# Kernel tuning notes

Hardware: AMD Instinct MI355X
Metric: run time of the kernel (lower is better)

The kernel has to match this reference:

```python
import jax, jax.numpy as jnp
import numpy as np

# dims
B, L = 2, 1024            # batch, seq len (queries == keys)
DQ, DK, DSRC = 1024, 1024, 512
VIEWS, WIDTH, TOPK = 8, 4, 8
DVP = DQ // VIEWS         # per-view head dim = 128
PAD_F = (WIDTH - 1) // 2  # dilocal 'same' zero padding (stride=1, dilation=1)
PAD_B = (WIDTH - 1) - PAD_F


def setup_inputs() -> dict:
    key = jax.random.key(0)
    ks = jax.random.split(key, 5)
    s = 0.02
    return {
        "query": jax.random.normal(ks[0], (B, L, DQ), jnp.float32),
        "key_t": jax.random.normal(ks[1], (B, L, DK), jnp.float32),
        "source": jax.random.normal(ks[2], (B, L, DSRC), jnp.float32),
        "wq": jax.random.normal(ks[3], (VIEWS, DVP, DQ), jnp.float32) * s,
        "bq": jnp.zeros((VIEWS, DVP), jnp.float32),
        "wk": jax.random.normal(ks[4], (VIEWS, DVP, DK), jnp.float32) * s,
        "bk": jnp.zeros((VIEWS, DVP), jnp.float32),
    }


def reference(query, key_t, source, wq, bq, wk, bk):
    # --- ViewPointFactory.forward ---
    # multi-view projections: [B, L, D] -> [B, views, L, dvp]
    q = jnp.einsum('bld,vkd->bvlk', query, wq) + bq[None, :, None, :]
    k = jnp.einsum('bld,vkd->bvlk', key_t, wk) + bk[None, :, None, :]
    # attention scores over all keys: [B, views, Lq, Lk] (no sqrt(d) scaling in source)
    score = jnp.einsum('bvqd,bvkd->bvqk', q, k)
    # torch.sort(descending) + slice == top_k with sorted values
    vals, idx = jax.lax.top_k(score, TOPK)          # [B, views, Lq, TOPK]
    weights = jax.nn.softmax(vals, axis=-1)

    # --- ViewPoint.__call__(source) ---
    # dilocal: width-WIDTH local windows, stride 1, dilation 1, zero 'same' pad
    padded = jnp.pad(source, ((0, 0), (PAD_F, PAD_B), (0, 0)))
    win_idx = jnp.arange(L)[:, None] + jnp.arange(WIDTH)[None, :]  # [L, WIDTH]
    windows = padded[:, win_idx, :]                 # [B, L, WIDTH, DSRC]

    # gather the top-k key windows per (view, query): [B, views, Lq, TOPK, WIDTH, DSRC]
    gathered = jax.vmap(lambda w, i: w[i])(windows, idx)
    # weighted sum over top-k -> [B, views, Lq, WIDTH, DSRC]
    out = jnp.einsum('bvqk,bvqkwd->bvqwd', weights, gathered)
    return out
```

## Files before the change

kernel.cpp:

```cpp
#include <hip/hip_runtime.h>
#include <cstdint>

#define L_SEQ 1024
#define DSRC 512
#define XPL 2097152L
#define WPL 1048576L

typedef __attribute__((ext_vector_type(8))) short short8;
typedef __attribute__((ext_vector_type(4))) float floatx4;

__device__ __forceinline__ unsigned short f2bf(float f) {
  unsigned int x = __float_as_uint(f);
  x += 0x7fff + ((x >> 16) & 1);
  return (unsigned short)(x >> 16);
}
__device__ __forceinline__ float bf2f(unsigned short h) {
  return __uint_as_float((unsigned)h << 16);
}
__device__ __forceinline__ void split3(float f, unsigned short* h) {
  h[0] = f2bf(f);
  float d = f - bf2f(h[0]);
  h[1] = f2bf(d);
  h[2] = f2bf(d - bf2f(h[1]));
}

__device__ __forceinline__ void gload_lds16(const void* g, void* l) {
  __builtin_amdgcn_global_load_lds(
      (const __attribute__((address_space(1))) unsigned int*)g,
      (__attribute__((address_space(3))) unsigned int*)l, 16, 0, 0);
}

__global__ __launch_bounds__(256) void split_inputs_k(
    const float* __restrict__ query, const float* __restrict__ key_t,
    const float* __restrict__ wq, const float* __restrict__ wk,
    ushort* __restrict__ xs, ushort* __restrict__ wsp) {
  int blk = blockIdx.x;
  const float* in; ushort* out; long pl; int idx;
  if (blk < 2048)      { in = query; out = xs;           pl = XPL; idx = blk; }
  else if (blk < 4096) { in = key_t; out = xs + 3 * XPL; pl = XPL; idx = blk - 2048; }
  else if (blk < 5120) { in = wq;    out = wsp;          pl = WPL; idx = blk - 4096; }
  else                 { in = wk;    out = wsp + 3 * WPL; pl = WPL; idx = blk - 5120; }
  long e = (long)idx * 1024 + threadIdx.x * 4;
  float4 v = *(const float4*)(in + e);
  unsigned short h0[3], h1[3], h2[3], h3[3];
  split3(v.x, h0); split3(v.y, h1); split3(v.z, h2); split3(v.w, h3);
#pragma unroll
  for (int s = 0; s < 3; s++) {
    ushort4 u; u.x = h0[s]; u.y = h1[s]; u.z = h2[s]; u.w = h3[s];
    *(ushort4*)(out + s * pl + e) = u;
  }
}

__global__ __launch_bounds__(512, 2) void proj_gemm_k(
    const ushort* __restrict__ xs, const ushort* __restrict__ wsp,
    ushort* __restrict__ qs, ushort* __restrict__ ks,
    const float* __restrict__ bq, const float* __restrict__ bk) {
  __shared__ ushort As[2][3][4096];
  __shared__ ushort Bs[2][3][4096];
  int z = blockIdx.z;
  const ushort* Ab = xs + (long)z * 3 * XPL + (long)blockIdx.y * 128 * 1024;
  const ushort* Bb = wsp + (long)z * 3 * WPL + (long)blockIdx.x * 128 * 1024;

  int tid = threadIdx.x;
  int lane = tid & 63, wv = tid >> 6;
  int wm = wv >> 2, wn = wv & 3;
  int quad = lane >> 4, l16 = lane & 15;

  int sr = tid >> 2;
  int scq = (((tid & 3) ^ ((sr >> 1) & 3)) << 3);

  floatx4 acc[4][2] = {};

#pragma unroll
  for (int s = 0; s < 3; s++) {
    gload_lds16(Ab + (long)s * XPL + (long)sr * 1024 + scq, &As[0][s][wv * 512]);
    gload_lds16(Bb + (long)s * WPL + (long)sr * 1024 + scq, &Bs[0][s][wv * 512]);
  }
  __syncthreads();

  int cur = 0;
#pragma unroll 2
  for (int t = 0; t < 32; t++) {
    if (t < 31) {
      int k0 = (t + 1) * 32;
#pragma unroll
      for (int s = 0; s < 3; s++) {
        gload_lds16(Ab + (long)s * XPL + (long)sr * 1024 + k0 + scq, &As[cur ^ 1][s][wv * 512]);
        gload_lds16(Bb + (long)s * WPL + (long)sr * 1024 + k0 + scq, &Bs[cur ^ 1][s][wv * 512]);
      }
    }
    short8 af[3][4];
#pragma unroll
    for (int s = 0; s < 3; s++)
#pragma unroll
      for (int i = 0; i < 4; i++) {
        int row = wm * 64 + i * 16 + l16;
        int qa = (quad ^ ((row >> 1) & 3)) << 3;
        af[s][i] = *(const short8*)(&As[cur][s][row * 32 + qa]);
      }
#pragma unroll
    for (int j = 0; j < 2; j++) {
      int rowb = wn * 32 + j * 16 + l16;
      int boff = rowb * 32 + ((quad ^ ((rowb >> 1) & 3)) << 3);
      short8 b0 = *(const short8*)(&Bs[cur][0][boff]);
      short8 b1 = *(const short8*)(&Bs[cur][1][boff]);
      short8 b2 = *(const short8*)(&Bs[cur][2][boff]);
#pragma unroll
      for (int i = 0; i < 4; i++) {
        acc[i][j] = __builtin_amdgcn_mfma_f32_16x16x32_bf16(af[1][i], b1, acc[i][j], 0, 0, 0);
        acc[i][j] = __builtin_amdgcn_mfma_f32_16x16x32_bf16(af[0][i], b2, acc[i][j], 0, 0, 0);
        acc[i][j] = __builtin_amdgcn_mfma_f32_16x16x32_bf16(af[2][i], b0, acc[i][j], 0, 0, 0);
        acc[i][j] = __builtin_amdgcn_mfma_f32_16x16x32_bf16(af[0][i], b1, acc[i][j], 0, 0, 0);
        acc[i][j] = __builtin_amdgcn_mfma_f32_16x16x32_bf16(af[1][i], b0, acc[i][j], 0, 0, 0);
        acc[i][j] = __builtin_amdgcn_mfma_f32_16x16x32_bf16(af[0][i], b0, acc[i][j], 0, 0, 0);
      }
    }
    __syncthreads();
    cur ^= 1;
  }

  ushort* Ob = z ? ks : qs;
  const float* bias = z ? bk : bq;
#pragma unroll
  for (int j = 0; j < 2; j++) {
    int col = blockIdx.x * 128 + wn * 32 + j * 16 + l16;
    float bv = bias[col];
#pragma unroll
    for (int i = 0; i < 4; i++) {
#pragma unroll
      for (int r = 0; r < 4; r++) {
        long row = blockIdx.y * 128 + wm * 64 + i * 16 + quad * 4 + r;
        float val = acc[i][j][r] + bv;
        unsigned short h[3]; split3(val, h);
        long e = row * 1024 + col;
#pragma unroll
        for (int s = 0; s < 3; s++) Ob[s * XPL + e] = h[s];
      }
    }
  }
}

__global__ __launch_bounds__(512, 4) void score_gemm_k(
    const ushort* __restrict__ qs, const ushort* __restrict__ ks,
    float* __restrict__ S, int b) {
  __shared__ ushort As[3][4096];
  __shared__ ushort Bs[3][4096];
  int v = blockIdx.z;
  const ushort* Ab = qs + (long)b * 1048576 + v * 128 + (long)blockIdx.y * 131072;
  const ushort* Bb = ks + (long)b * 1048576 + v * 128 + (long)blockIdx.x * 131072;

  int tid = threadIdx.x;
  int lane = tid & 63, wv = tid >> 6;
  int wm = wv >> 2, wn = wv & 3;
  int quad = lane >> 4, l16 = lane & 15;

  int sr = tid >> 2;
  int scq = (((tid & 3) ^ ((sr >> 1) & 3)) << 3);

  floatx4 acc[4][2] = {};

  for (int t = 0; t < 4; t++) {
    int k0 = t * 32;
#pragma unroll
    for (int s = 0; s < 3; s++) {
      gload_lds16(Ab + (long)s * XPL + (long)sr * 1024 + k0 + scq, &As[s][wv * 512]);
      gload_lds16(Bb + (long)s * XPL + (long)sr * 1024 + k0 + scq, &Bs[s][wv * 512]);
    }
    __syncthreads();

    short8 af[3][4];
#pragma unroll
    for (int s = 0; s < 3; s++)
#pragma unroll
      for (int i = 0; i < 4; i++) {
        int row = wm * 64 + i * 16 + l16;
        int qa = (quad ^ ((row >> 1) & 3)) << 3;
        af[s][i] = *(const short8*)(&As[s][row * 32 + qa]);
      }
#pragma unroll
    for (int j = 0; j < 2; j++) {
      int rowb = wn * 32 + j * 16 + l16;
      int boff = rowb * 32 + ((quad ^ ((rowb >> 1) & 3)) << 3);
      short8 b0 = *(const short8*)(&Bs[0][boff]);
      short8 b1 = *(const short8*)(&Bs[1][boff]);
      short8 b2 = *(const short8*)(&Bs[2][boff]);
#pragma unroll
      for (int i = 0; i < 4; i++) {
        acc[i][j] = __builtin_amdgcn_mfma_f32_16x16x32_bf16(af[1][i], b1, acc[i][j], 0, 0, 0);
        acc[i][j] = __builtin_amdgcn_mfma_f32_16x16x32_bf16(af[0][i], b2, acc[i][j], 0, 0, 0);
        acc[i][j] = __builtin_amdgcn_mfma_f32_16x16x32_bf16(af[2][i], b0, acc[i][j], 0, 0, 0);
        acc[i][j] = __builtin_amdgcn_mfma_f32_16x16x32_bf16(af[0][i], b1, acc[i][j], 0, 0, 0);
        acc[i][j] = __builtin_amdgcn_mfma_f32_16x16x32_bf16(af[1][i], b0, acc[i][j], 0, 0, 0);
        acc[i][j] = __builtin_amdgcn_mfma_f32_16x16x32_bf16(af[0][i], b0, acc[i][j], 0, 0, 0);
      }
    }
    __syncthreads();
  }

  float* Sb = S + (long)v * 1048576;
#pragma unroll
  for (int j = 0; j < 2; j++) {
    int col = blockIdx.x * 128 + wn * 32 + j * 16 + l16;
#pragma unroll
    for (int i = 0; i < 4; i++) {
#pragma unroll
      for (int r = 0; r < 4; r++) {
        int row = blockIdx.y * 128 + wm * 64 + i * 16 + quad * 4 + r;
        Sb[(long)row * 1024 + col] = acc[i][j][r];
      }
    }
  }
}

__global__ __launch_bounds__(256) void topk_softmax_k(const float* __restrict__ scores,
                                                      float* __restrict__ wts,
                                                      int* __restrict__ idxs) {
  int row = blockIdx.x * 4 + (threadIdx.x >> 6);
  int lane = threadIdx.x & 63;
  const float4* s4 = (const float4*)(scores + (long)row * 1024);
  float v[16];
#pragma unroll
  for (int i = 0; i < 4; i++) {
    float4 t4 = s4[i * 64 + lane];
    v[i * 4 + 0] = t4.x; v[i * 4 + 1] = t4.y; v[i * 4 + 2] = t4.z; v[i * 4 + 3] = t4.w;
  }
  float topv[8]; int topi[8];
  for (int t = 0; t < 8; t++) {
    float bv = -1e30f; int bi = 1 << 30; int bslot = -1;
#pragma unroll
    for (int i = 0; i < 16; i++) {
      int ci = ((i >> 2) << 8) + (lane << 2) + (i & 3);
      if (v[i] > bv) { bv = v[i]; bi = ci; bslot = i; }
    }
    float rv = bv; int ri = bi;
    for (int off = 32; off; off >>= 1) {
      float ov = __shfl_down(rv, off);
      int oi = __shfl_down(ri, off);
      if (ov > rv || (ov == rv && oi < ri)) { rv = ov; ri = oi; }
    }
    rv = __shfl(rv, 0); ri = __shfl(ri, 0);
    topv[t] = rv; topi[t] = ri;
    if (bslot >= 0 && bi == ri) v[bslot] = -1e30f;
  }
  float m = topv[0], sum = 0.f, e[8];
#pragma unroll
  for (int t = 0; t < 8; t++) { e[t] = __expf(topv[t] - m); sum += e[t]; }
  float inv = 1.0f / sum;
  if (lane < 8) {
    wts[(long)row * 8 + lane] = e[lane] * inv;
    idxs[(long)row * 8 + lane] = topi[lane];
  }
}

__global__ __launch_bounds__(256) void gather_out_k(const float* __restrict__ src,
                                                    const float* __restrict__ wts,
                                                    const int* __restrict__ idxs,
                                                    float* __restrict__ out) {
  int rowid = blockIdx.x;
  int b = rowid >> 13;
  int tid = threadIdx.x;
  int d4 = tid & 127;
  int w0 = (tid >> 7) << 1;
  const float4* s4 = (const float4*)src + (long)b * (L_SEQ * (DSRC / 4));
  float wt[8]; int id[8];
#pragma unroll
  for (int k = 0; k < 8; k++) {
    wt[k] = wts[(long)rowid * 8 + k];
    id[k] = idxs[(long)rowid * 8 + k];
  }
  float ax = 0, ay = 0, az = 0, aw = 0;
  float bx = 0, by = 0, bz2 = 0, bw = 0;
#pragma unroll
  for (int k = 0; k < 8; k++) {
    int r0 = id[k] + w0 - 1;
    if ((unsigned)r0 < (unsigned)L_SEQ) {
      float4 x = s4[(long)r0 * 128 + d4];
      ax += wt[k] * x.x; ay += wt[k] * x.y; az += wt[k] * x.z; aw += wt[k] * x.w;
    }
    int r1 = r0 + 1;
    if ((unsigned)r1 < (unsigned)L_SEQ) {
      float4 x = s4[(long)r1 * 128 + d4];
      bx += wt[k] * x.x; by += wt[k] * x.y; bz2 += wt[k] * x.z; bw += wt[k] * x.w;
    }
  }
  float4* o4 = (float4*)out + ((long)rowid * 4 + w0) * 128 + d4;
  o4[0] = make_float4(ax, ay, az, aw);
  o4[128] = make_float4(bx, by, bz2, bw);
}

extern "C" void kernel_launch(void* const* d_in, const int* in_sizes, int n_in,
                              void* d_out, int out_size, void* d_ws, size_t ws_size,
                              hipStream_t stream) {
  (void)in_sizes; (void)n_in; (void)out_size; (void)ws_size;
  const float* query  = (const float*)d_in[0];
  const float* key_t  = (const float*)d_in[1];
  const float* source = (const float*)d_in[2];
  const float* wq     = (const float*)d_in[3];
  const float* bq     = (const float*)d_in[4];
  const float* wk     = (const float*)d_in[5];
  const float* bk     = (const float*)d_in[6];

  char* ws = (char*)d_ws;
  ushort* qs  = (ushort*)(ws);
  ushort* ksp = (ushort*)(ws + 12582912);
  float*  wts = (float*)(ws + 25165824);
  int*    idxs= (int*)(ws + 25690112);
  ushort* xs  = (ushort*)(ws + 26214400);
  ushort* wsp = (ushort*)(ws + 51380224);
  float*  sc  = (float*)(ws + 26214400);

  split_inputs_k<<<6144, 256, 0, stream>>>(query, key_t, wq, wk, xs, wsp);
  proj_gemm_k<<<dim3(8, 16, 2), 512, 0, stream>>>(xs, wsp, qs, ksp, bq, bk);
  for (int b = 0; b < 2; b++) {
    score_gemm_k<<<dim3(8, 8, 8), 512, 0, stream>>>(qs, ksp, sc, b);
    topk_softmax_k<<<2048, 256, 0, stream>>>(sc, wts + (long)b * 65536, idxs + b * 65536);
  }
  gather_out_k<<<16384, 256, 0, stream>>>(source, wts, idxs, (float*)d_out);
}
```

Measured before the change: 328.8 us.

## Fuse score GEMM with streaming top-k softmax, avoiding score matrix round-trip

Replaces the per-batch score GEMM plus separate top-k/softmax kernels with one kernel. Each block keeps a 64-row query tile resident in LDS and streams key tiles through a double-buffered LDS stage. After each 128-column tile it keeps a running top-8 per row via shuffle merges, so the full 8x1024x1024 fp32 score matrix is never written to or read from global memory. Blocks are mapped to XCDs by (batch, view) pair. The cost is fewer, heavier blocks (256 total), larger LDS use, and serial top-k merge work interleaved between MFMA phases.

```diff
diff --git a/kernel.cpp b/kernel.cpp
--- a/kernel.cpp
+++ b/kernel.cpp
@@ -140,116 +140,170 @@
   }
 }
 
-__global__ __launch_bounds__(512, 4) void score_gemm_k(
+__global__ __launch_bounds__(512) void score_topk_k(
     const ushort* __restrict__ qs, const ushort* __restrict__ ks,
-    float* __restrict__ S, int b) {
-  __shared__ ushort As[3][4096];
-  __shared__ ushort Bs[3][4096];
-  int v = blockIdx.z;
-  const ushort* Ab = qs + (long)b * 1048576 + v * 128 + (long)blockIdx.y * 131072;
-  const ushort* Bb = ks + (long)b * 1048576 + v * 128 + (long)blockIdx.x * 131072;
+    float* __restrict__ wts, int* __restrict__ idxs) {
+  __shared__ ushort Asm[3 * 64 * 128];
+  __shared__ ushort Bsm[2][3 * 128 * 32];
+  __shared__ float  Ssm[64 * 132];
+
+  int fid = blockIdx.x + 16 * (blockIdx.y + 8 * blockIdx.z);
+  int xcd = fid & 7, jj = fid >> 3;
+  int pair = xcd * 2 + (jj & 1);
+  int rt = jj >> 1;
+  int v = pair & 7, b = pair >> 3;
+
+  const long arow0 = (long)b * 1024 + rt * 64;
+  const long brow0 = (long)b * 1024;
+  const int vb = v * 128;
 
   int tid = threadIdx.x;
   int lane = tid & 63, wv = tid >> 6;
   int wm = wv >> 2, wn = wv & 3;
   int quad = lane >> 4, l16 = lane & 15;
 
-  int sr = tid >> 2;
-  int scq = (((tid & 3) ^ ((sr >> 1) & 3)) << 3);
-
-  floatx4 acc[4][2] = {};
-
-  for (int t = 0; t < 4; t++) {
-    int k0 = t * 32;
-#pragma unroll
-    for (int s = 0; s < 3; s++) {
-      gload_lds16(Ab + (long)s * XPL + (long)sr * 1024 + k0 + scq, &As[s][wv * 512]);
-      gload_lds16(Bb + (long)s * XPL + (long)sr * 1024 + k0 + scq, &Bs[s][wv * 512]);
-    }
+#pragma unroll
+  for (int n = 0; n < 6; n++) {
+    int base = n * 512 + wv * 64;
+    int sl = base + lane;
+    int s = sl >> 10, rem = sl & 1023;
+    int r = rem >> 4, sq = rem & 15;
+    int qb = sq ^ (r & 7);
+    gload_lds16(qs + (long)s * XPL + (arow0 + r) * 1024 + vb + qb * 8,
+                &Asm[base * 8]);
+  }
+
+  auto stageB = [&](int step, int bsel) {
+    int ct2 = step >> 2, kk2 = step & 3;
+    long kb = brow0 + ct2 * 128;
+    int k0 = kk2 * 32;
+#pragma unroll
+    for (int n = 0; n < 3; n++) {
+      int base = n * 512 + wv * 64;
+      int sl = base + lane;
+      int s = sl >> 9, rem = sl & 511;
+      int c = rem >> 2, sq = rem & 3;
+      int qb = sq ^ ((c >> 1) & 3);
+      gload_lds16(ks + (long)s * XPL + (kb + c) * 1024 + vb + k0 + qb * 8,
+                  &Bsm[bsel][base * 8]);
+    }
+  };
+
+  stageB(0, 0);
+  __syncthreads();
+
+  floatx4 acc[2][2] = {};
+  float rv = -1e30f; int rc = 0x7FFFFFFF;
+  const int myrow = tid >> 3, lc = tid & 7;
+
+  int buf = 0;
+  for (int ct = 0; ct < 8; ct++) {
+#pragma unroll
+    for (int kk = 0; kk < 4; kk++) {
+      int step = ct * 4 + kk;
+      if (step < 31) stageB(step + 1, buf ^ 1);
+
+      short8 af[3][2], bf[3][2];
+#pragma unroll
+      for (int s = 0; s < 3; s++)
+#pragma unroll
+        for (int i = 0; i < 2; i++) {
+          int row = wm * 32 + i * 16 + l16;
+          int sqa = (kk * 4 + quad) ^ (row & 7);
+          af[s][i] = *(const short8*)(&Asm[s * 8192 + row * 128 + sqa * 8]);
+        }
+#pragma unroll
+      for (int s = 0; s < 3; s++)
+#pragma unroll
+        for (int j = 0; j < 2; j++) {
+          int c = wn * 32 + j * 16 + l16;
+          int sqb = quad ^ ((c >> 1) & 3);
+          bf[s][j] = *(const short8*)(&Bsm[buf][s * 4096 + c * 32 + sqb * 8]);
+        }
+#pragma unroll
+      for (int j = 0; j < 2; j++)
+#pragma unroll
+        for (int i = 0; i < 2; i++) {
+          acc[i][j] = __builtin_amdgcn_mfma_f32_16x16x32_bf16(af[1][i], bf[1][j], acc[i][j], 0, 0, 0);
+          acc[i][j] = __builtin_amdgcn_mfma_f32_16x16x32_bf16(af[0][i], bf[2][j], acc[i][j], 0, 0, 0);
+          acc[i][j] = __builtin_amdgcn_mfma_f32_16x16x32_bf16(af[2][i], bf[0][j], acc[i][j], 0, 0, 0);
+          acc[i][j] = __builtin_amdgcn_mfma_f32_16x16x32_bf16(af[0][i], bf[1][j], acc[i][j], 0, 0, 0);
+          acc[i][j] = __builtin_amdgcn_mfma_f32_16x16x32_bf16(af[1][i], bf[0][j], acc[i][j], 0, 0, 0);
+          acc[i][j] = __builtin_amdgcn_mfma_f32_16x16x32_bf16(af[0][i], bf[0][j], acc[i][j], 0, 0, 0);
+        }
+      __syncthreads();
+      buf ^= 1;
+    }
+
+#pragma unroll
+    for (int i = 0; i < 2; i++)
+#pragma unroll
+      for (int j = 0; j < 2; j++)
+#pragma unroll
+        for (int r = 0; r < 4; r++) {
+          int row = wm * 32 + i * 16 + quad * 4 + r;
+          int col = wn * 32 + j * 16 + l16;
+          Ssm[row * 132 + col] = acc[i][j][r];
+          acc[i][j][r] = 0.0f;
+        }
     __syncthreads();
 
-    short8 af[3][4];
-#pragma unroll
-    for (int s = 0; s < 3; s++)
-#pragma unroll
-      for (int i = 0; i < 4; i++) {
-        int row = wm * 64 + i * 16 + l16;
-        int qa = (quad ^ ((row >> 1) & 3)) << 3;
-        af[s][i] = *(const short8*)(&As[s][row * 32 + qa]);
-      }
-#pragma unroll
-    for (int j = 0; j < 2; j++) {
-      int rowb = wn * 32 + j * 16 + l16;
-      int boff = rowb * 32 + ((quad ^ ((rowb >> 1) & 3)) << 3);
-      short8 b0 = *(const short8*)(&Bs[0][boff]);
-      short8 b1 = *(const short8*)(&Bs[1][boff]);
-      short8 b2 = *(const short8*)(&Bs[2][boff]);
-#pragma unroll
-      for (int i = 0; i < 4; i++) {
-        acc[i][j] = __builtin_amdgcn_mfma_f32_16x16x32_bf16(af[1][i], b1, acc[i][j], 0, 0, 0);
-        acc[i][j] = __builtin_amdgcn_mfma_f32_16x16x32_bf16(af[0][i], b2, acc[i][j], 0, 0, 0);
-        acc[i][j] = __builtin_amdgcn_mfma_f32_16x16x32_bf16(af[2][i], b0, acc[i][j], 0, 0, 0);
-        acc[i][j] = __builtin_amdgcn_mfma_f32_16x16x32_bf16(af[0][i], b1, acc[i][j], 0, 0, 0);
-        acc[i][j] = __builtin_amdgcn_mfma_f32_16x16x32_bf16(af[1][i], b0, acc[i][j], 0, 0, 0);
-        acc[i][j] = __builtin_amdgcn_mfma_f32_16x16x32_bf16(af[0][i], b0, acc[i][j], 0, 0, 0);
-      }
-    }
-    __syncthreads();
-  }
-
-  float* Sb = S + (long)v * 1048576;
-#pragma unroll
-  for (int j = 0; j < 2; j++) {
-    int col = blockIdx.x * 128 + wn * 32 + j * 16 + l16;
-#pragma unroll
-    for (int i = 0; i < 4; i++) {
-#pragma unroll
-      for (int r = 0; r < 4; r++) {
-        int row = blockIdx.y * 128 + wm * 64 + i * 16 + quad * 4 + r;
-        Sb[(long)row * 1024 + col] = acc[i][j][r];
-      }
-    }
-  }
-}
-
-__global__ __launch_bounds__(256) void topk_softmax_k(const float* __restrict__ scores,
-                                                      float* __restrict__ wts,
-                                                      int* __restrict__ idxs) {
-  int row = blockIdx.x * 4 + (threadIdx.x >> 6);
-  int lane = threadIdx.x & 63;
-  const float4* s4 = (const float4*)(scores + (long)row * 1024);
-  float v[16];
-#pragma unroll
-  for (int i = 0; i < 4; i++) {
-    float4 t4 = s4[i * 64 + lane];
-    v[i * 4 + 0] = t4.x; v[i * 4 + 1] = t4.y; v[i * 4 + 2] = t4.z; v[i * 4 + 3] = t4.w;
-  }
-  float topv[8]; int topi[8];
-  for (int t = 0; t < 8; t++) {
-    float bv = -1e30f; int bi = 1 << 30; int bslot = -1;
-#pragma unroll
-    for (int i = 0; i < 16; i++) {
-      int ci = ((i >> 2) << 8) + (lane << 2) + (i & 3);
-      if (v[i] > bv) { bv = v[i]; bi = ci; bslot = i; }
-    }
-    float rv = bv; int ri = bi;
-    for (int off = 32; off; off >>= 1) {
-      float ov = __shfl_down(rv, off);
-      int oi = __shfl_down(ri, off);
-      if (ov > rv || (ov == rv && oi < ri)) { rv = ov; ri = oi; }
-    }
-    rv = __shfl(rv, 0); ri = __shfl(ri, 0);
-    topv[t] = rv; topi[t] = ri;
-    if (bslot >= 0 && bi == ri) v[bslot] = -1e30f;
-  }
-  float m = topv[0], sum = 0.f, e[8];
-#pragma unroll
-  for (int t = 0; t < 8; t++) { e[t] = __expf(topv[t] - m); sum += e[t]; }
-  float inv = 1.0f / sum;
-  if (lane < 8) {
-    wts[(long)row * 8 + lane] = e[lane] * inv;
-    idxs[(long)row * 8 + lane] = topi[lane];
-  }
+    float vv[16];
+#pragma unroll
+    for (int t = 0; t < 16; t++) vv[t] = Ssm[myrow * 132 + lc + 8 * t];
+
+    float nv = -1e30f; int nc = 0x7FFFFFFF;
+    for (int rd = 0; rd < 8; rd++) {
+      float bv = -1e30f; int bs = 0;
+#pragma unroll
+      for (int t = 0; t < 16; t++)
+        if (vv[t] > bv) { bv = vv[t]; bs = t; }
+      int bc = ct * 128 + lc + 8 * bs;
+      int myc = bc;
+#pragma unroll
+      for (int m = 1; m <= 4; m <<= 1) {
+        float ov = __shfl_xor(bv, m);
+        int oc = __shfl_xor(bc, m);
+        if (ov > bv || (ov == bv && oc < bc)) { bv = ov; bc = oc; }
+      }
+      if (myc == bc) {
+#pragma unroll
+        for (int t = 0; t < 16; t++)
+          if (t == bs) vv[t] = -1e30f;
+      }
+      if (lc == rd) { nv = bv; nc = bc; }
+    }
+
+    float orv = -1e30f; int orc = 0x7FFFFFFF;
+    for (int rd = 0; rd < 8; rd++) {
+      float bv; int bc;
+      if (rv > nv || (rv == nv && rc < nc)) { bv = rv; bc = rc; }
+      else { bv = nv; bc = nc; }
+#pragma unroll
+      for (int m = 1; m <= 4; m <<= 1) {
+        float ov = __shfl_xor(bv, m);
+        int oc = __shfl_xor(bc, m);
+        if (ov > bv || (ov == bv && oc < bc)) { bv = ov; bc = oc; }
+      }
+      if (bc == rc) rv = -1e30f;
+      else if (bc == nc) nv = -1e30f;
+      if (lc == rd) { orv = bv; orc = bc; }
+    }
+    rv = orv; rc = orc;
+  }
+
+  float mm = rv;
+#pragma unroll
+  for (int m = 1; m <= 4; m <<= 1) mm = fmaxf(mm, __shfl_xor(mm, m));
+  float e = __expf(rv - mm);
+  float sum = e;
+#pragma unroll
+  for (int m = 1; m <= 4; m <<= 1) sum += __shfl_xor(sum, m);
+  float w = e * (1.0f / sum);
+
+  long grow = (long)b * 8192 + v * 1024 + rt * 64 + myrow;
+  wts[grow * 8 + lc] = w;
+  idxs[grow * 8 + lc] = rc;
 }
 
 __global__ __launch_bounds__(256) void gather_out_k(const float* __restrict__ src,
@@ -307,13 +361,9 @@
   int*    idxs= (int*)(ws + 25690112);
   ushort* xs  = (ushort*)(ws + 26214400);
   ushort* wsp = (ushort*)(ws + 51380224);
-  float*  sc  = (float*)(ws + 26214400);
 
   split_inputs_k<<<6144, 256, 0, stream>>>(query, key_t, wq, wk, xs, wsp);
   proj_gemm_k<<<dim3(8, 16, 2), 512, 0, stream>>>(xs, wsp, qs, ksp, bq, bk);
-  for (int b = 0; b < 2; b++) {
-    score_gemm_k<<<dim3(8, 8, 8), 512, 0, stream>>>(qs, ksp, sc, b);
-    topk_softmax_k<<<2048, 256, 0, stream>>>(sc, wts + (long)b * 65536, idxs + b * 65536);
-  }
+  score_topk_k<<<dim3(16, 8, 2), 512, 0, stream>>>(qs, ksp, wts, idxs);
   gather_out_k<<<16384, 256, 0, stream>>>(source, wts, idxs, (float*)d_out);
 }
```

Measured after the change: 336.0 us. 2.2% more time.
